# Performance work log

Hardware: AMD Instinct MI355X
Metric: run time of the kernel (lower is better)

Reference implementation:

```python
import jax, jax.numpy as jnp
import numpy as np

R = 128          # input voxel grid resolution
N = 200000
C_IN = 128
C_OUT = 256
G = 32           # group-norm groups
EPS = 1e-5


def _build_sparse_structure():
    """Generate random sparse voxel coords, downsample map, and 3x3x3 neighbor table."""
    rng = np.random.default_rng(0)
    lin = rng.choice(R ** 3, size=N, replace=False)
    cx, cy, cz = lin // (R * R), (lin // R) % R, lin % R
    # downsample by 2: coords // 2 on a (R//2)^3 grid
    Rd = R // 2
    key = ((cx // 2) * Rd + (cy // 2)) * Rd + (cz // 2)
    uk, inv = np.unique(key, return_inverse=True)   # uk sorted
    M = len(uk)
    dx, dy, dz = uk // (Rd * Rd), (uk // Rd) % Rd, uk % Rd
    # 27-neighbor table for submanifold 3x3x3 conv on the downsampled coords
    nbr = np.full((M, 27), -1, np.int32)
    k = 0
    for ox in (-1, 0, 1):
        for oy in (-1, 0, 1):
            for oz in (-1, 0, 1):
                nx, ny, nz = dx + ox, dy + oy, dz + oz
                valid = (nx >= 0) & (nx < Rd) & (ny >= 0) & (ny < Rd) & (nz >= 0) & (nz < Rd)
                nkey = (nx * Rd + ny) * Rd + nz
                pos = np.clip(np.searchsorted(uk, nkey), 0, M - 1)
                found = valid & (uk[pos] == nkey)
                nbr[:, k] = np.where(found, pos, -1).astype(np.int32)
                k += 1
    return inv.astype(np.int32), nbr, M


def setup_inputs() -> dict:
    pool_seg, nbr_idx, M = _build_sparse_structure()
    key = jax.random.key(0)
    ks = jax.random.split(key, 12)
    f32 = jnp.float32
    feats = jax.random.normal(ks[0], (N, C_IN), f32)
    s1 = float(1.0 / np.sqrt(27 * C_IN))
    s2 = float(1.0 / np.sqrt(27 * C_OUT))
    return {
        "feats": feats,
        "gn1_w": 1.0 + 0.1 * jax.random.normal(ks[1], (C_IN,), f32),
        "gn1_b": 0.1 * jax.random.normal(ks[2], (C_IN,), f32),
        "W1": jax.random.normal(ks[3], (27, C_IN, C_OUT), f32) * s1,
        "b1": 0.01 * jax.random.normal(ks[4], (C_OUT,), f32),
        "gn2_w": 1.0 + 0.1 * jax.random.normal(ks[5], (C_OUT,), f32),
        "gn2_b": 0.1 * jax.random.normal(ks[6], (C_OUT,), f32),
        "W2": jax.random.normal(ks[7], (27, C_OUT, C_OUT), f32) * s2,
        "b2": 0.01 * jax.random.normal(ks[8], (C_OUT,), f32),
        "Wskip": jax.random.normal(ks[9], (C_IN, C_OUT), f32) * float(1.0 / np.sqrt(C_IN)),
        "bskip": 0.01 * jax.random.normal(ks[10], (C_OUT,), f32),
        "pool_seg": jnp.asarray(pool_seg),
        "nbr_idx": jnp.asarray(nbr_idx),
        "num_down": int(M),
    }


def _group_norm(x, gamma, beta):
    # batch size 1: normalize each group over all voxels and its channels
    n, c = x.shape
    xg = x.reshape(n, G, c // G)
    mu = xg.mean(axis=(0, 2), keepdims=True)
    var = xg.var(axis=(0, 2), keepdims=True)
    xn = (xg - mu) * jax.lax.rsqrt(var + EPS)
    return xn.reshape(n, c) * gamma + beta


def _sparse_conv3(x, W, b, nbr_idx):
    # submanifold 3x3x3 conv: out[i] = sum_k W[k] @ x[nbr[i,k]] (missing nbr -> 0)
    idx = jnp.maximum(nbr_idx, 0)
    mask = (nbr_idx >= 0).astype(x.dtype)
    acc = jnp.zeros((x.shape[0], W.shape[2]), x.dtype)
    for k in range(27):
        acc = acc + (x[idx[:, k]] * mask[:, k:k + 1]) @ W[k]
    return acc + b


def reference(feats, gn1_w, gn1_b, W1, b1, gn2_w, gn2_b, W2, b2, Wskip, bskip,
              pool_seg, nbr_idx, num_down):
    # act_layers: GroupNorm32 + SiLU on the full-resolution sparse tensor
    h = jax.nn.silu(_group_norm(feats, gn1_w, gn1_b))
    # SparseDownsample(2): average features of voxels sharing a coord//2 cell
    cnt = jax.ops.segment_sum(jnp.ones((feats.shape[0], 1), feats.dtype),
                              pool_seg, num_segments=num_down)
    inv_cnt = 1.0 / jnp.maximum(cnt, 1.0)
    h_d = jax.ops.segment_sum(h, pool_seg, num_segments=num_down) * inv_cnt
    x_d = jax.ops.segment_sum(feats, pool_seg, num_segments=num_down) * inv_cnt
    # out_layers: conv3 -> GN -> SiLU -> conv3
    h1 = _sparse_conv3(h_d, W1, b1, nbr_idx)
    h2 = jax.nn.silu(_group_norm(h1, gn2_w, gn2_b))
    h3 = _sparse_conv3(h2, W2, b2, nbr_idx)
    # skip: 1x1 sparse conv on downsampled input, then add (same coord set)
    skip = x_d @ Wskip + bskip
    return h3 + skip
```

## Files before the change

kernel.cpp:

```cpp
#include <hip/hip_runtime.h>
#include <hip/hip_bf16.h>
#include <stdint.h>

typedef __hip_bfloat16 bf16;
typedef __attribute__((ext_vector_type(8))) __bf16 bf16x8;
typedef __attribute__((ext_vector_type(4))) float f32x4;
typedef __attribute__((ext_vector_type(4))) int i32x4;

#define GN_EPS 1e-5f

__device__ __forceinline__ float silu_f(float x) {
  return x / (1.f + __expf(-x));
}

__device__ __forceinline__ float ldf(const void* p, size_t i, int f) {
  return f ? ((const float*)p)[i]
           : __bfloat162float(((const bf16*)p)[i]);
}

__device__ __forceinline__ void llds16(const void* g, void* l) {
  __builtin_amdgcn_global_load_lds(
      (const __attribute__((address_space(1))) unsigned int*)g,
      (__attribute__((address_space(3))) unsigned int*)l, 16, 0, 0);
}

__global__ void detect_k(const void* __restrict__ gn1w, int* __restrict__ flag) {
  if (threadIdx.x == 0 && blockIdx.x == 0) {
    const unsigned short* u = (const unsigned short*)gn1w;
    float mx = 0.f;
    for (int i = 0; i < 128; ++i) {
      unsigned int b = ((unsigned int)u[i]) << 16;
      float v = __uint_as_float(b);
      v = fabsf(v);
      if (!isnan(v) && v > mx) mx = v;
    }
    flag[0] = (mx > 1e4f) ? 1 : 0;
  }
}

__global__ void transpose_k(const void* __restrict__ in, bf16* __restrict__ out,
                            int CI, int CO, const int* __restrict__ flagp) {
  const int f = *flagp;
  int k = blockIdx.y;
  int ntco = CO >> 5;
  int tci = blockIdx.x / ntco, tco = blockIdx.x % ntco;
  __shared__ float t[32][33];
  int tx = threadIdx.x & 31, ty = threadIdx.x >> 5;
  size_t base = (size_t)k * CI * CO;
  bf16* dst = out + base;
#pragma unroll
  for (int j = 0; j < 4; ++j)
    t[ty + 8 * j][tx] =
        ldf(in, base + (size_t)(tci * 32 + ty + 8 * j) * CO + tco * 32 + tx, f);
  __syncthreads();
#pragma unroll
  for (int j = 0; j < 4; ++j)
    dst[(size_t)(tco * 32 + ty + 8 * j) * CI + tci * 32 + tx] =
        __float2bfloat16(t[tx][ty + 8 * j]);
}

__global__ void gn_stats_k(const void* __restrict__ x, float* __restrict__ raw,
                           int rows, int C, const int* __restrict__ flagp) {
  const int f = *flagp;
  int tid = threadIdx.x;
  int rpb = 256 / C;
  int c = tid & (C - 1);
  int stripe = tid / C;
  float s = 0.f, sq = 0.f;
  for (int r = blockIdx.x * rpb + stripe; r < rows; r += gridDim.x * rpb) {
    float v = ldf(x, (size_t)r * C + c, f);
    s += v; sq += v * v;
  }
  __shared__ float ls[256], lq[256];
  ls[tid] = s; lq[tid] = sq;
  __syncthreads();
  if (tid < 32) {
    int per = C >> 5;
    float as = 0.f, aq = 0.f;
    for (int st = 0; st < rpb; ++st)
      for (int e = 0; e < per; ++e) {
        int idx = st * C + tid * per + e;
        as += ls[idx]; aq += lq[idx];
      }
    atomicAdd(&raw[tid], as);
    atomicAdd(&raw[32 + tid], aq);
  }
}

__global__ void gn_fin_k(const float* __restrict__ raw, float* __restrict__ fin,
                         float count) {
  int g = threadIdx.x;
  if (g < 32) {
    float mu = raw[g] / count;
    float var = fmaxf(raw[32 + g] / count - mu * mu, 0.f);
    fin[g] = mu;
    fin[32 + g] = rsqrtf(var + GN_EPS);
  }
}

__global__ void slots_k(const int* __restrict__ seg, int* __restrict__ cnt,
                        int* __restrict__ slots, int N) {
  int i = blockIdx.x * 256 + threadIdx.x;
  if (i >= N) return;
  int s = seg[i];
  int p = atomicAdd(&cnt[s], 1);
  if (p < 8) slots[s * 8 + p] = i;
}

__global__ void down_k(const void* __restrict__ feats, const int* __restrict__ slots,
                       const int* __restrict__ cnt, const float* __restrict__ fin1,
                       const void* __restrict__ gw, const void* __restrict__ gb,
                       bf16* __restrict__ xd, bf16* __restrict__ hd, int M,
                       const int* __restrict__ flagp) {
  const int f = *flagp;
  int cell = blockIdx.x * 2 + (threadIdx.x >> 7);
  int c = threadIdx.x & 127;
  if (cell >= M) return;
  int n = min(cnt[cell], 8);
  int g = c >> 2;
  float mu = fin1[g], is = fin1[32 + g];
  float w = ldf(gw, c, f), b = ldf(gb, c, f);
  float xs = 0.f, hs = 0.f;
  for (int j = 0; j < n; ++j) {
    int v = slots[cell * 8 + j];
    float fv = ldf(feats, (size_t)v * 128 + c, f);
    xs += fv;
    hs += silu_f((fv - mu) * is * w + b);
  }
  float inv = 1.f / (float)max(n, 1);
  xd[(size_t)cell * 128 + c] = __float2bfloat16(xs * inv);
  hd[(size_t)cell * 128 + c] = __float2bfloat16(hs * inv);
}

__global__ void act2_k(bf16* __restrict__ h, const float* __restrict__ fin2,
                       const void* __restrict__ gw, const void* __restrict__ gb,
                       size_t total8, const int* __restrict__ flagp) {
  const int f = *flagp;
  size_t i = (size_t)blockIdx.x * 256 + threadIdx.x;
  if (i >= total8) return;
  int c0 = (int)((i * 8) & 255);
  int g = c0 >> 3;
  float mu = fin2[g], is = fin2[32 + g];
  bf16x8 v = *reinterpret_cast<bf16x8*>(h + i * 8);
  bf16x8 o;
#pragma unroll
  for (int j = 0; j < 8; ++j) {
    float x = (float)v[j];
    float t = (x - mu) * is * ldf(gw, c0 + j, f) + ldf(gb, c0 + j, f);
    o[j] = (__bf16)silu_f(t);
  }
  *reinterpret_cast<bf16x8*>(h + i * 8) = o;
}

template <int CIN, bool SKIP>
__global__ __launch_bounds__(256, 2) void conv_k(
    const bf16* __restrict__ A, const bf16* __restrict__ Wt,
    const void* __restrict__ bias, const void* __restrict__ bias2,
    const bf16* __restrict__ Xd, const int* __restrict__ nbr,
    void* __restrict__ out, int M, int nwg, const void* __restrict__ zp,
    const int* __restrict__ biasflagp, const int* __restrict__ outflagp) {
  constexpr int NCB = CIN / 64;
  constexpr int NT = 27 * NCB + (SKIP ? 2 : 0);
  __shared__ alignas(16) char smem[2 * 32768];

  const int bflag = *biasflagp, oflag = *outflagp;
  const int tid = threadIdx.x;
  const int wave = tid >> 6, lane = tid & 63;

  int bid = blockIdx.x;
  int q = nwg >> 3, r8 = nwg & 7, xcd = bid & 7, ix = bid >> 3;
  int wg = (xcd < r8 ? xcd * (q + 1) : r8 * (q + 1) + (xcd - r8) * q) + ix;
  const int row0 = (wg >> 1) * 128, n0 = (wg & 1) * 128;

  const int rb8 = lane >> 3;
  const int slot = lane & 7;
  const int gc = slot ^ rb8;
  const int mrow = lane & 15, quad = lane >> 4;
  const int wr = wave >> 1, wc = wave & 1;

  auto nbr_fetch = [&](int t) -> i32x4 {
    i32x4 s;
    bool isW = (!SKIP) || (t < 27 * NCB);
    int kk = isW ? (t / NCB) : 0;
#pragma unroll
    for (int ro = 0; ro < 4; ++ro) {
      int g = row0 + ro * 32 + wave * 8 + rb8;
      int v = -1;
      if (isW) {
        if (g < M) v = nbr[(size_t)g * 27 + kk];
      } else {
        if (g < M) v = g;
      }
      s[ro] = v;
    }
    return s;
  };

  auto stage = [&](int t, char* buf, i32x4 srcs) {
    bool isW = (!SKIP) || (t < 27 * NCB);
    int cb = isW ? (t % NCB) : (t - 27 * NCB);
    int cink = isW ? CIN : 128;
    const bf16* Ab = isW ? A : Xd;
    const bf16* Wb = Wt + (isW ? (size_t)(t / NCB) * (256 * CIN)
                               : (size_t)27 * (256 * CIN));
    const int coff = cb * 64 + gc * 8;
#pragma unroll
    for (int ro = 0; ro < 4; ++ro) {
      int rrow = ro * 32 + wave * 8 + rb8;
      int src = srcs[ro];
      const bf16* ga = (src >= 0) ? Ab + (size_t)src * cink + coff
                                  : (const bf16*)zp;
      const bf16* gw2 = Wb + (size_t)(n0 + rrow) * cink + coff;
      char* la = buf + ro * 4096 + wave * 1024;
      char* lb = buf + 16384 + ro * 4096 + wave * 1024;
      llds16(ga, la);
      llds16(gw2, lb);
    }
  };

  f32x4 acc[4][4] = {};

  i32x4 sN = nbr_fetch(0);
  stage(0, smem, sN);
  sN = nbr_fetch(1);
  asm volatile("s_waitcnt vmcnt(0)" ::: "memory");
  __builtin_amdgcn_s_barrier();

#pragma unroll 2
  for (int t = 0; t < NT; ++t) {
    char* cur = smem + (t & 1) * 32768;
    if (t + 1 < NT) stage(t + 1, smem + ((t + 1) & 1) * 32768, sN);
    if (t + 2 < NT) sN = nbr_fetch(t + 2);
    const char* sA = cur + (size_t)(wr * 64 + mrow) * 128;
    const char* sB = cur + 16384 + (size_t)(wc * 64 + mrow) * 128;
#pragma unroll
    for (int ks = 0; ks < 2; ++ks) {
      const int co = ((ks * 4 + quad) ^ (mrow & 7)) * 16;
      bf16x8 af[4], bv[4];
#pragma unroll
      for (int i = 0; i < 4; ++i)
        af[i] = *reinterpret_cast<const bf16x8*>(sA + i * (16 * 128) + co);
#pragma unroll
      for (int j = 0; j < 4; ++j)
        bv[j] = *reinterpret_cast<const bf16x8*>(sB + j * (16 * 128) + co);
      __builtin_amdgcn_s_setprio(1);
#pragma unroll
      for (int i = 0; i < 4; ++i)
#pragma unroll
        for (int j = 0; j < 4; ++j)
          acc[i][j] = __builtin_amdgcn_mfma_f32_16x16x32_bf16(af[i], bv[j],
                                                              acc[i][j], 0, 0, 0);
      __builtin_amdgcn_s_setprio(0);
    }
    asm volatile("s_waitcnt vmcnt(0)" ::: "memory");
    __builtin_amdgcn_s_barrier();
  }

#pragma unroll
  for (int j = 0; j < 4; ++j) {
    int col = n0 + wc * 64 + j * 16 + mrow;
    float bvl = ldf(bias, col, bflag);
    if (SKIP) bvl += ldf(bias2, col, bflag);
#pragma unroll
    for (int i = 0; i < 4; ++i) {
      int rb = row0 + wr * 64 + i * 16 + quad * 4;
#pragma unroll
      for (int r = 0; r < 4; ++r) {
        int row = rb + r;
        if (row < M) {
          size_t idx = (size_t)row * 256 + col;
          float val = acc[i][j][r] + bvl;
          if (oflag) ((float*)out)[idx] = val;
          else ((bf16*)out)[idx] = __float2bfloat16(val);
        }
      }
    }
  }
}

extern "C" void kernel_launch(void* const* d_in, const int* in_sizes, int n_in,
                              void* d_out, int out_size, void* d_ws, size_t ws_size,
                              hipStream_t stream) {
  const void* feats = d_in[0];
  const void* gn1w = d_in[1];
  const void* gn1b = d_in[2];
  const void* W1 = d_in[3];
  const void* b1 = d_in[4];
  const void* gn2w = d_in[5];
  const void* gn2b = d_in[6];
  const void* W2 = d_in[7];
  const void* b2 = d_in[8];
  const void* Wsk = d_in[9];
  const void* bsk = d_in[10];
  const int* pool = (const int*)d_in[11];
  const int* nbr = (const int*)d_in[12];
  const int N = in_sizes[0] / 128;
  const int M = out_size / 256;

  char* ws = (char*)d_ws;
  auto aup = [](size_t x) { return (x + 255) & ~(size_t)255; };
  float* raw1 = (float*)(ws + 0);
  float* raw2 = (float*)(ws + 256);
  int* flag = (int*)(ws + 512);
  int* zeroflag = (int*)(ws + 516);
  const void* zp = (const void*)(ws + 768);
  int* cnt = (int*)(ws + 1024);
  size_t o = aup(1024 + (size_t)M * 4);
  float* fin1 = (float*)(ws + o); o += 256;
  float* fin2 = (float*)(ws + o); o += 256;
  int* slots = (int*)(ws + o); o = aup(o + (size_t)M * 32);
  bf16* xd = (bf16*)(ws + o); o += (size_t)M * 256;
  bf16* hd = (bf16*)(ws + o); o += (size_t)M * 256;
  bf16* h1 = (bf16*)(ws + o); o += (size_t)M * 512;
  bf16* wt1 = (bf16*)(ws + o); o += (size_t)27 * 256 * 128 * 2;
  bf16* wt2 = (bf16*)(ws + o); o += ((size_t)27 * 256 * 256 + 256 * 128) * 2;
  (void)ws_size; (void)n_in;

  hipMemsetAsync(ws, 0, 1024 + (size_t)M * 4, stream);

  detect_k<<<1, 64, 0, stream>>>(gn1w, flag);

  transpose_k<<<dim3(4 * 8, 27), 256, 0, stream>>>(W1, wt1, 128, 256, flag);
  transpose_k<<<dim3(8 * 8, 27), 256, 0, stream>>>(W2, wt2, 256, 256, flag);
  transpose_k<<<dim3(4 * 8, 1), 256, 0, stream>>>(
      Wsk, wt2 + (size_t)27 * 256 * 256, 128, 256, flag);

  gn_stats_k<<<512, 256, 0, stream>>>(feats, raw1, N, 128, flag);
  gn_fin_k<<<1, 64, 0, stream>>>(raw1, fin1, (float)N * 4.f);

  slots_k<<<(N + 255) / 256, 256, 0, stream>>>(pool, cnt, slots, N);
  down_k<<<(M + 1) / 2, 256, 0, stream>>>(feats, slots, cnt, fin1, gn1w, gn1b,
                                          xd, hd, M, flag);

  const int nby = (M + 127) / 128;
  const int nwg = 2 * nby;

  conv_k<128, false><<<nwg, 256, 0, stream>>>(
      hd, wt1, b1, nullptr, nullptr, nbr, h1, M, nwg, zp, flag, zeroflag);

  gn_stats_k<<<512, 256, 0, stream>>>(h1, raw2, M, 256, zeroflag);
  gn_fin_k<<<1, 64, 0, stream>>>(raw2, fin2, (float)M * 8.f);
  act2_k<<<(int)(((size_t)M * 32 + 255) / 256), 256, 0, stream>>>(
      h1, fin2, gn2w, gn2b, (size_t)M * 32, flag);

  conv_k<256, true><<<nwg, 256, 0, stream>>>(
      h1, wt2, b2, bsk, xd, nbr, d_out, M, nwg, zp, flag, flag);
}
```

Before: 1.494 ms.

## Restructure sparse conv into 192x256 tiles with 4-stage LDS ring and cached neighbor table

The sparse conv kernel now uses 512-thread blocks that each compute a 192-row by full 256-column output tile, so the gathered activation rows are loaded once rather than by two column blocks. The K step drops to 32 channels and uses a 4-deep LDS ring with explicit per-wave vmcnt waits, keeping three stages in flight. The 27-entry neighbor indices for the tile are preloaded into shared memory once. In exchange, LDS use grows to about 140KB per block, which may limit occupancy, and each thread holds more accumulator registers.

```diff
diff --git a/kernel.cpp b/kernel.cpp
--- a/kernel.cpp
+++ b/kernel.cpp
@@ -5,7 +5,6 @@
 typedef __hip_bfloat16 bf16;
 typedef __attribute__((ext_vector_type(8))) __bf16 bf16x8;
 typedef __attribute__((ext_vector_type(4))) float f32x4;
-typedef __attribute__((ext_vector_type(4))) int i32x4;
 
 #define GN_EPS 1e-5f
 
@@ -153,15 +152,19 @@
 }
 
 template <int CIN, bool SKIP>
-__global__ __launch_bounds__(256, 2) void conv_k(
+__global__ __launch_bounds__(512, 2) void conv_k(
     const bf16* __restrict__ A, const bf16* __restrict__ Wt,
     const void* __restrict__ bias, const void* __restrict__ bias2,
     const bf16* __restrict__ Xd, const int* __restrict__ nbr,
     void* __restrict__ out, int M, int nwg, const void* __restrict__ zp,
     const int* __restrict__ biasflagp, const int* __restrict__ outflagp) {
-  constexpr int NCB = CIN / 64;
-  constexpr int NT = 27 * NCB + (SKIP ? 2 : 0);
-  __shared__ alignas(16) char smem[2 * 32768];
+  constexpr int NCB = CIN / 32;
+  constexpr int LOG_NCB = (CIN == 256) ? 3 : 2;
+  constexpr int NT = 27 * NCB + (SKIP ? 4 : 0);
+  __shared__ alignas(16) char smem[49152 + 65536 + 27648];
+  char* Aring = smem;
+  char* Bring = smem + 49152;
+  int* nbrT = (int*)(smem + 49152 + 65536);
 
   const int bflag = *biasflagp, oflag = *outflagp;
   const int tid = threadIdx.x;
@@ -170,100 +173,120 @@
   int bid = blockIdx.x;
   int q = nwg >> 3, r8 = nwg & 7, xcd = bid & 7, ix = bid >> 3;
   int wg = (xcd < r8 ? xcd * (q + 1) : r8 * (q + 1) + (xcd - r8) * q) + ix;
-  const int row0 = (wg >> 1) * 128, n0 = (wg & 1) * 128;
-
-  const int rb8 = lane >> 3;
-  const int slot = lane & 7;
-  const int gc = slot ^ rb8;
+  const int row0 = wg * 192;
+
+  for (int i = tid; i < 27 * 256; i += 512) {
+    int k = i >> 8, r = i & 255;
+    int g = row0 + r;
+    int v = -1;
+    if (r < 192 && g < M) v = nbr[(size_t)g * 27 + k];
+    nbrT[i] = v;
+  }
+  __syncthreads();
+
+  const int srow = lane >> 2;
+  const int schk = lane & 3;
+
+  auto stage = [&](int t) {
+    char* Asl = Aring + (size_t)(t & 3) * 12288;
+    char* Bsl = Bring + (size_t)(t & 3) * 16384;
+    const bool isW = (!SKIP) || (t < 27 * NCB);
+    const int kk = t >> LOG_NCB;
+    const int cb = isW ? (t & (NCB - 1)) : (t - 27 * NCB);
+    const int cink = isW ? CIN : 128;
+    const bf16* Ab = isW ? A : Xd;
+    const bf16* Wb = Wt + (isW ? (size_t)kk * (256 * CIN)
+                               : (size_t)27 * (256 * CIN));
+    const int koff = cb * 32;
+#pragma unroll
+    for (int ro = 0; ro < 2; ++ro) {
+      int c = ro * 128 + wave * 16 + srow;
+      int lc = schk ^ ((c >> 1) & 3);
+      llds16(Wb + (size_t)c * cink + koff + lc * 8,
+             Bsl + (size_t)(ro * 128 + wave * 16) * 64);
+    }
+    {
+      int r = wave * 16 + srow;
+      int src;
+      if (isW) src = nbrT[(kk << 8) + r];
+      else { int g = row0 + r; src = (g < M) ? g : -1; }
+      int lc = schk ^ ((r >> 1) & 3);
+      const bf16* ga = (src >= 0) ? Ab + (size_t)src * cink + koff + lc * 8
+                                  : (const bf16*)zp;
+      llds16(ga, Asl + (size_t)(wave * 16) * 64);
+    }
+    if (wave < 4) {
+      int r = 128 + wave * 16 + srow;
+      int src;
+      if (isW) src = nbrT[(kk << 8) + r];
+      else { int g = row0 + r; src = (g < M) ? g : -1; }
+      int lc = schk ^ ((r >> 1) & 3);
+      const bf16* ga = (src >= 0) ? Ab + (size_t)src * cink + koff + lc * 8
+                                  : (const bf16*)zp;
+      llds16(ga, Asl + (size_t)(128 + wave * 16) * 64);
+    }
+  };
+
   const int mrow = lane & 15, quad = lane >> 4;
-  const int wr = wave >> 1, wc = wave & 1;
-
-  auto nbr_fetch = [&](int t) -> i32x4 {
-    i32x4 s;
-    bool isW = (!SKIP) || (t < 27 * NCB);
-    int kk = isW ? (t / NCB) : 0;
-#pragma unroll
-    for (int ro = 0; ro < 4; ++ro) {
-      int g = row0 + ro * 32 + wave * 8 + rb8;
-      int v = -1;
-      if (isW) {
-        if (g < M) v = nbr[(size_t)g * 27 + kk];
-      } else {
-        if (g < M) v = g;
-      }
-      s[ro] = v;
-    }
-    return s;
+  const int wr = wave >> 2, wc = wave & 3;
+  const int cswz = (quad ^ ((mrow >> 1) & 3)) * 16;
+
+  f32x4 acc[6][4] = {};
+
+  auto compute = [&](int t) {
+    const char* As = Aring + (size_t)(t & 3) * 12288 +
+                     (size_t)(wr * 96 + mrow) * 64 + cswz;
+    const char* Bs = Bring + (size_t)(t & 3) * 16384 +
+                     (size_t)(wc * 64 + mrow) * 64 + cswz;
+    bf16x8 af[6], bv[4];
+#pragma unroll
+    for (int i = 0; i < 6; ++i)
+      af[i] = *reinterpret_cast<const bf16x8*>(As + i * (16 * 64));
+#pragma unroll
+    for (int j = 0; j < 4; ++j)
+      bv[j] = *reinterpret_cast<const bf16x8*>(Bs + j * (16 * 64));
+    __builtin_amdgcn_s_setprio(1);
+#pragma unroll
+    for (int i = 0; i < 6; ++i)
+#pragma unroll
+      for (int j = 0; j < 4; ++j)
+        acc[i][j] = __builtin_amdgcn_mfma_f32_16x16x32_bf16(af[i], bv[j],
+                                                            acc[i][j], 0, 0, 0);
+    __builtin_amdgcn_s_setprio(0);
   };
 
-  auto stage = [&](int t, char* buf, i32x4 srcs) {
-    bool isW = (!SKIP) || (t < 27 * NCB);
-    int cb = isW ? (t % NCB) : (t - 27 * NCB);
-    int cink = isW ? CIN : 128;
-    const bf16* Ab = isW ? A : Xd;
-    const bf16* Wb = Wt + (isW ? (size_t)(t / NCB) * (256 * CIN)
-                               : (size_t)27 * (256 * CIN));
-    const int coff = cb * 64 + gc * 8;
-#pragma unroll
-    for (int ro = 0; ro < 4; ++ro) {
-      int rrow = ro * 32 + wave * 8 + rb8;
-      int src = srcs[ro];
-      const bf16* ga = (src >= 0) ? Ab + (size_t)src * cink + coff
-                                  : (const bf16*)zp;
-      const bf16* gw2 = Wb + (size_t)(n0 + rrow) * cink + coff;
-      char* la = buf + ro * 4096 + wave * 1024;
-      char* lb = buf + 16384 + ro * 4096 + wave * 1024;
-      llds16(ga, la);
-      llds16(gw2, lb);
-    }
-  };
-
-  f32x4 acc[4][4] = {};
-
-  i32x4 sN = nbr_fetch(0);
-  stage(0, smem, sN);
-  sN = nbr_fetch(1);
-  asm volatile("s_waitcnt vmcnt(0)" ::: "memory");
-  __builtin_amdgcn_s_barrier();
-
-#pragma unroll 2
-  for (int t = 0; t < NT; ++t) {
-    char* cur = smem + (t & 1) * 32768;
-    if (t + 1 < NT) stage(t + 1, smem + ((t + 1) & 1) * 32768, sN);
-    if (t + 2 < NT) sN = nbr_fetch(t + 2);
-    const char* sA = cur + (size_t)(wr * 64 + mrow) * 128;
-    const char* sB = cur + 16384 + (size_t)(wc * 64 + mrow) * 128;
-#pragma unroll
-    for (int ks = 0; ks < 2; ++ks) {
-      const int co = ((ks * 4 + quad) ^ (mrow & 7)) * 16;
-      bf16x8 af[4], bv[4];
-#pragma unroll
-      for (int i = 0; i < 4; ++i)
-        af[i] = *reinterpret_cast<const bf16x8*>(sA + i * (16 * 128) + co);
-#pragma unroll
-      for (int j = 0; j < 4; ++j)
-        bv[j] = *reinterpret_cast<const bf16x8*>(sB + j * (16 * 128) + co);
-      __builtin_amdgcn_s_setprio(1);
-#pragma unroll
-      for (int i = 0; i < 4; ++i)
-#pragma unroll
-        for (int j = 0; j < 4; ++j)
-          acc[i][j] = __builtin_amdgcn_mfma_f32_16x16x32_bf16(af[i], bv[j],
-                                                              acc[i][j], 0, 0, 0);
-      __builtin_amdgcn_s_setprio(0);
-    }
-    asm volatile("s_waitcnt vmcnt(0)" ::: "memory");
-    __builtin_amdgcn_s_barrier();
-  }
+#define VMW(a, b)                                                      \
+  do {                                                                 \
+    if (wave < 4) asm volatile("s_waitcnt vmcnt(" #a ")" ::: "memory"); \
+    else          asm volatile("s_waitcnt vmcnt(" #b ")" ::: "memory"); \
+  } while (0)
+#define BAR() asm volatile("s_barrier" ::: "memory")
+
+  stage(0); stage(1); stage(2);
+
+#pragma unroll 1
+  for (int t = 0; t < NT - 3; ++t) {
+    stage(t + 3);
+    VMW(12, 9);
+    BAR();
+    compute(t);
+    BAR();
+  }
+  VMW(8, 6); BAR(); compute(NT - 3); BAR();
+  VMW(4, 3); BAR(); compute(NT - 2); BAR();
+  VMW(0, 0); BAR(); compute(NT - 1);
+
+#undef VMW
+#undef BAR
 
 #pragma unroll
   for (int j = 0; j < 4; ++j) {
-    int col = n0 + wc * 64 + j * 16 + mrow;
+    int col = wc * 64 + j * 16 + mrow;
     float bvl = ldf(bias, col, bflag);
     if (SKIP) bvl += ldf(bias2, col, bflag);
 #pragma unroll
-    for (int i = 0; i < 4; ++i) {
-      int rb = row0 + wr * 64 + i * 16 + quad * 4;
+    for (int i = 0; i < 6; ++i) {
+      int rb = row0 + wr * 96 + i * 16 + quad * 4;
 #pragma unroll
       for (int r = 0; r < 4; ++r) {
         int row = rb + r;
@@ -332,10 +355,9 @@
   down_k<<<(M + 1) / 2, 256, 0, stream>>>(feats, slots, cnt, fin1, gn1w, gn1b,
                                           xd, hd, M, flag);
 
-  const int nby = (M + 127) / 128;
-  const int nwg = 2 * nby;
-
-  conv_k<128, false><<<nwg, 256, 0, stream>>>(
+  const int nwg = (M + 191) / 192;
+
+  conv_k<128, false><<<nwg, 512, 0, stream>>>(
       hd, wt1, b1, nullptr, nullptr, nbr, h1, M, nwg, zp, flag, zeroflag);
 
   gn_stats_k<<<512, 256, 0, stream>>>(h1, raw2, M, 256, zeroflag);
@@ -343,6 +365,6 @@
   act2_k<<<(int)(((size_t)M * 32 + 255) / 256), 256, 0, stream>>>(
       h1, fin2, gn2w, gn2b, (size_t)M * 32, flag);
 
-  conv_k<256, true><<<nwg, 256, 0, stream>>>(
+  conv_k<256, true><<<nwg, 512, 0, stream>>>(
       h1, wt2, b2, bsk, xd, nbr, d_out, M, nwg, zp, flag, flag);
 }
```

Result: no change. 1.479 ms (-1.0%).
